# Kernel optimization log

Hardware: AMD Instinct MI355X
Metric: run time of the kernel (lower is better)

## Reference

```python
import jax, jax.numpy as jnp
from jax import lax
import numpy as np

D_STATE = 16
D_CONV = 4
GROUPS = 4
TOKEN = 8


def group_norm(x, w, b, groups, eps=1e-5):
    # x: [B, C, H, W]; torch GroupNorm semantics
    B, C, H, W = x.shape
    xg = x.reshape(B, groups, C // groups, H, W)
    mu = xg.mean(axis=(2, 3, 4), keepdims=True)
    var = ((xg - mu) ** 2).mean(axis=(2, 3, 4), keepdims=True)
    xg = (xg - mu) / jnp.sqrt(var + eps)
    return xg.reshape(B, C, H, W) * w[None, :, None, None] + b[None, :, None, None]


def mamba_fwd(x, in_w, conv_w, conv_b, xproj_w, dt_w, dt_b, A_log, D, out_w):
    # x: [B, L, d_model]. Faithful mamba_ssm Mamba forward (no biases on in/out proj).
    Bsz, L, _ = x.shape
    d_inner = in_w.shape[0] // 2
    dt_rank = dt_w.shape[1]
    xz = x @ in_w.T                                   # [B, L, 2*d_inner]
    xi, z = jnp.split(xz, 2, axis=-1)
    # causal depthwise conv1d (kernel D_CONV) + SiLU
    xc = lax.conv_general_dilated(
        xi.transpose(0, 2, 1), conv_w, window_strides=(1,),
        padding=[(D_CONV - 1, 0)], dimension_numbers=("NCH", "OIH", "NCH"),
        feature_group_count=d_inner)
    xc = jax.nn.silu(xc + conv_b[None, :, None]).transpose(0, 2, 1)  # [B, L, d_inner]
    xdb = xc @ xproj_w.T                               # [B, L, dt_rank + 2*d_state]
    dt, Bm, Cm = jnp.split(xdb, [dt_rank, dt_rank + D_STATE], axis=-1)
    dt = jax.nn.softplus(dt @ dt_w.T + dt_b)           # [B, L, d_inner]
    A = -jnp.exp(A_log)                                # [d_inner, d_state]
    dA = jnp.exp(dt[..., None] * A)                    # [B, L, d_inner, d_state]
    dBx = dt[..., None] * Bm[:, :, None, :] * xc[..., None]

    def step(h, inp):
        dA_t, dBx_t, C_t = inp                         # [B,di,ds],[B,di,ds],[B,ds]
        h = dA_t * h + dBx_t
        y = jnp.einsum('bds,bs->bd', h, C_t)
        return h, y

    h0 = jnp.zeros((Bsz, d_inner, D_STATE), dtype=x.dtype)
    _, ys = lax.scan(step, h0, (dA.transpose(1, 0, 2, 3),
                                dBx.transpose(1, 0, 2, 3),
                                Cm.transpose(1, 0, 2)))
    y = ys.transpose(1, 0, 2) + xc * D                 # skip term D*x
    y = y * jax.nn.silu(z)
    return y @ out_w.T


def setup_inputs() -> dict:
    key = jax.random.key(0)
    ks = iter(jax.random.split(key, 48))

    def rn(shape, s=0.02):
        return jax.random.normal(next(ks), shape, dtype=jnp.float32) * s

    B, C, H, W = 4, 64, 64, 64
    inp = {"x": jax.random.normal(next(ks), (B, C, H, W), dtype=jnp.float32)}

    def mamba_params(prefix, d_model):
        d_inner = 2 * d_model
        dt_rank = -(-d_model // 16)
        inp[prefix + "_in_w"] = rn((2 * d_inner, d_model))
        inp[prefix + "_conv_w"] = rn((d_inner, 1, D_CONV))
        inp[prefix + "_conv_b"] = rn((d_inner,))
        inp[prefix + "_xproj_w"] = rn((dt_rank + 2 * D_STATE, d_inner))
        inp[prefix + "_dt_w"] = rn((d_inner, dt_rank))
        inp[prefix + "_dt_b"] = rn((d_inner,)) + 0.5
        inp[prefix + "_A_log"] = jnp.log(jnp.tile(jnp.arange(1, D_STATE + 1, dtype=jnp.float32), (d_inner, 1)))
        inp[prefix + "_D"] = jnp.ones((d_inner,), jnp.float32)
        inp[prefix + "_out_w"] = rn((d_model, d_inner))

    mamba_params("spa", C)
    mamba_params("spe", -(-C // TOKEN))  # group_channel_num = ceil(64/8) = 8
    inp["spa_gn_w"] = jnp.ones((C,), jnp.float32)
    inp["spa_gn_b"] = jnp.zeros((C,), jnp.float32)
    inp["spe_gn_w"] = jnp.ones((C,), jnp.float32)
    inp["spe_gn_b"] = jnp.zeros((C,), jnp.float32)
    inp["att_w"] = jnp.full((2,), 0.5, jnp.float32)
    return inp


def reference(x,
              spa_in_w, spa_conv_w, spa_conv_b, spa_xproj_w, spa_dt_w, spa_dt_b,
              spa_A_log, spa_D, spa_out_w,
              spe_in_w, spe_conv_w, spe_conv_b, spe_xproj_w, spe_dt_w, spe_dt_b,
              spe_A_log, spe_D, spe_out_w,
              spa_gn_w, spa_gn_b, spe_gn_w, spe_gn_b, att_w):
    B, C, H, W = x.shape
    gcn = -(-C // TOKEN)  # C == TOKEN*gcn here, so no padding path is taken

    # --- SpaMamba: flatten all pixels into one sequence [1, B*H*W, C] ---
    xs = x.transpose(0, 2, 3, 1).reshape(1, -1, C)
    ys = mamba_fwd(xs, spa_in_w, spa_conv_w, spa_conv_b, spa_xproj_w,
                   spa_dt_w, spa_dt_b, spa_A_log, spa_D, spa_out_w)
    ys = ys.reshape(B, H, W, C).transpose(0, 3, 1, 2)
    spa = jax.nn.silu(group_norm(ys, spa_gn_w, spa_gn_b, GROUPS)) + x

    # --- SpeMamba: per-pixel spectral tokens [B*H*W, TOKEN, gcn] ---
    xe = x.transpose(0, 2, 3, 1).reshape(B * H * W, TOKEN, gcn)
    ye = mamba_fwd(xe, spe_in_w, spe_conv_w, spe_conv_b, spe_xproj_w,
                   spe_dt_w, spe_dt_b, spe_A_log, spe_D, spe_out_w)
    ye = ye.reshape(B, H, W, C).transpose(0, 3, 1, 2)
    spe = x + jax.nn.silu(group_norm(ye, spe_gn_w, spe_gn_b, GROUPS))

    w = jax.nn.softmax(att_w)
    return spa * w[0] + spe * w[1] + x
```

## Files before the change

kernel.cpp:

```cpp
#include <hip/hip_runtime.h>

__device__ __forceinline__ float siluf(float x){ return x / (1.f + __expf(-x)); }
__device__ __forceinline__ float softplusf(float x){
    return fmaxf(x, 0.f) + __logf(1.f + __expf(-fabsf(x)));
}
#if __has_builtin(__builtin_amdgcn_exp2f)
__device__ __forceinline__ float fexp2(float x){ return __builtin_amdgcn_exp2f(x); }
#else
__device__ __forceinline__ float fexp2(float x){ return exp2f(x); }
#endif

__global__ void __launch_bounds__(256) k_inproj_conv(const float* __restrict__ x,
        const float* __restrict__ in_w, const float* __restrict__ cw, const float* __restrict__ cb,
        float* __restrict__ xc, float* __restrict__ zb){
    __shared__ float sxe[11][68];
    int tid = threadIdx.x;
    int l0 = blockIdx.x * 8;
    #pragma unroll
    for (int it = 0; it < 3; ++it){
        int idx = it*256 + tid;
        if (idx < 704){
            int r = idx >> 6, c = idx & 63;
            int p = l0 - 3 + r;
            float v = 0.f;
            if (p >= 0) v = x[(size_t)(p >> 12)*262144 + c*4096 + (p & 4095)];
            sxe[r][c] = v;
        }
    }
    float wr[64];
    const float4* w4 = (const float4*)(in_w + tid*64);
    #pragma unroll
    for (int k = 0; k < 16; ++k){
        float4 v = w4[k];
        wr[4*k]=v.x; wr[4*k+1]=v.y; wr[4*k+2]=v.z; wr[4*k+3]=v.w;
    }
    __syncthreads();
    if (tid < 128){
        float acc[11];
        #pragma unroll
        for (int r = 0; r < 11; ++r) acc[r] = 0.f;
        #pragma unroll
        for (int k = 0; k < 16; ++k){
            #pragma unroll
            for (int r = 0; r < 11; ++r){
                float4 v = *(const float4*)&sxe[r][4*k];
                acc[r] = fmaf(v.x, wr[4*k],   acc[r]);
                acc[r] = fmaf(v.y, wr[4*k+1], acc[r]);
                acc[r] = fmaf(v.z, wr[4*k+2], acc[r]);
                acc[r] = fmaf(v.w, wr[4*k+3], acc[r]);
            }
        }
        float cw0 = cw[tid*4+0], cw1 = cw[tid*4+1], cw2 = cw[tid*4+2], cw3 = cw[tid*4+3];
        float cbd = cb[tid];
        #pragma unroll
        for (int r = 0; r < 8; ++r){
            float a = fmaf(cw0, acc[r],   cbd);
            a = fmaf(cw1, acc[r+1], a);
            a = fmaf(cw2, acc[r+2], a);
            a = fmaf(cw3, acc[r+3], a);
            xc[(size_t)(l0+r)*128 + tid] = siluf(a);
        }
    } else {
        float acc[8];
        #pragma unroll
        for (int r = 0; r < 8; ++r) acc[r] = 0.f;
        #pragma unroll
        for (int k = 0; k < 16; ++k){
            #pragma unroll
            for (int r = 0; r < 8; ++r){
                float4 v = *(const float4*)&sxe[r+3][4*k];
                acc[r] = fmaf(v.x, wr[4*k],   acc[r]);
                acc[r] = fmaf(v.y, wr[4*k+1], acc[r]);
                acc[r] = fmaf(v.z, wr[4*k+2], acc[r]);
                acc[r] = fmaf(v.w, wr[4*k+3], acc[r]);
            }
        }
        int dz = tid - 128;
        #pragma unroll
        for (int r = 0; r < 8; ++r) zb[(size_t)(l0+r)*128 + dz] = acc[r];
    }
}

__global__ void __launch_bounds__(256) k_scan_p1(const float* __restrict__ xc,
        const float* __restrict__ xpw, const float* __restrict__ dtw, const float* __restrict__ dtb,
        const float* __restrict__ A_log, float* __restrict__ Pb, float* __restrict__ Qb){
    __shared__ float sxc[2048];
    __shared__ float sbm[256];
    __shared__ __align__(16) float dtr[64];
    const int tid = threadIdx.x;
    const int ch = blockIdx.x;
    {
        const float4* src = (const float4*)(xc + (size_t)ch*2048);
        float4* dst = (float4*)sxc;
        dst[tid] = src[tid];
        dst[256 + tid] = src[256 + tid];
    }
    __syncthreads();
    {
        int j = tid & 63, tg = tid >> 6;
        if (j < 20){
            const float4* w4  = (const float4*)(xpw + j*128);
            const float4* xc4 = (const float4*)sxc + tg*128;
            float acc[4];
            #pragma unroll
            for (int r = 0; r < 4; ++r) acc[r] = 0.f;
            #pragma unroll 8
            for (int k = 0; k < 32; ++k){
                float4 w = w4[k];
                #pragma unroll
                for (int r = 0; r < 4; ++r){
                    float4 v = xc4[r*32 + k];
                    acc[r] = fmaf(v.x, w.x, acc[r]);
                    acc[r] = fmaf(v.y, w.y, acc[r]);
                    acc[r] = fmaf(v.z, w.z, acc[r]);
                    acc[r] = fmaf(v.w, w.w, acc[r]);
                }
            }
            if (j < 4){
                #pragma unroll
                for (int r = 0; r < 4; ++r) dtr[(tg*4+r)*4 + j] = acc[r];
            } else {
                #pragma unroll
                for (int r = 0; r < 4; ++r) sbm[(tg*4+r)*16 + (j-4)] = acc[r];
            }
        }
    }
    __syncthreads();
    const int d  = tid & 127;
    const int sh = tid >> 7;
    float A8[8];
    {
        const float4* al4 = (const float4*)(A_log + d*16 + sh*8);
        float4 v0 = al4[0], v1 = al4[1];
        A8[0]=-__expf(v0.x)*1.44269504f; A8[1]=-__expf(v0.y)*1.44269504f;
        A8[2]=-__expf(v0.z)*1.44269504f; A8[3]=-__expf(v0.w)*1.44269504f;
        A8[4]=-__expf(v1.x)*1.44269504f; A8[5]=-__expf(v1.y)*1.44269504f;
        A8[6]=-__expf(v1.z)*1.44269504f; A8[7]=-__expf(v1.w)*1.44269504f;
    }
    float4 dw = *(const float4*)(dtw + d*4);
    float dbd = dtb[d];
    float P[8], Q[8];
    #pragma unroll
    for (int s = 0; s < 8; ++s){ P[s] = 1.f; Q[s] = 0.f; }
    #pragma unroll 4
    for (int i = 0; i < 16; ++i){
        float4 dt4 = *(const float4*)(dtr + i*4);
        float dv = dbd;
        dv = fmaf(dt4.x, dw.x, dv);
        dv = fmaf(dt4.y, dw.y, dv);
        dv = fmaf(dt4.z, dw.z, dv);
        dv = fmaf(dt4.w, dw.w, dv);
        float dt = softplusf(dv);
        float db = dt * sxc[i*128 + d];
        const float4* bmr = (const float4*)(sbm + i*16 + sh*8);
        float4 b0 = bmr[0], b1 = bmr[1];
        float bv[8] = {b0.x,b0.y,b0.z,b0.w,b1.x,b1.y,b1.z,b1.w};
        #pragma unroll
        for (int s = 0; s < 8; ++s){
            float a = fexp2(dt*A8[s]);
            P[s] *= a;
            Q[s] = fmaf(a, Q[s], db*bv[s]);
        }
    }
    float* Pp = Pb + (size_t)ch*2048 + d*16 + sh*8;
    float* Qp = Qb + (size_t)ch*2048 + d*16 + sh*8;
    ((float4*)Pp)[0] = make_float4(P[0],P[1],P[2],P[3]);
    ((float4*)Pp)[1] = make_float4(P[4],P[5],P[6],P[7]);
    ((float4*)Qp)[0] = make_float4(Q[0],Q[1],Q[2],Q[3]);
    ((float4*)Qp)[1] = make_float4(Q[4],Q[5],Q[6],Q[7]);
}

#define XE_   0
#define XCL_  1216
#define BCL_  3904
#define DTV_  8640
#define SPG_  8768
#define WEIN_ 8800
#define WECW_ 9056
#define WECB_ 9120
#define WEAL_ 9136
#define WDTW_ 9392
#define WDTB_ 9408
#define WDV_  9424
__global__ void __launch_bounds__(256) k_spe(
        const float* __restrict__ x,
        const float* __restrict__ ein_w, const float* __restrict__ ecw, const float* __restrict__ ecb,
        const float* __restrict__ expw, const float* __restrict__ edtw, const float* __restrict__ edtb,
        const float* __restrict__ eA_log, const float* __restrict__ eDv, const float* __restrict__ eow,
        float* __restrict__ ye, float* __restrict__ sp)
{
    __shared__ float smem[9440];
    const int tid = threadIdx.x;
    const int pix = tid >> 4;
    const int d   = tid & 15;
    const int eb  = blockIdx.x;
    const int p0  = eb * 16;
    const int b   = p0 >> 12;
    const int hw0 = p0 & 4095;

    #pragma unroll
    for (int it = 0; it < 3; ++it){
        int idx = it*256 + tid;
        if (idx < 640){
            float v;
            if      (idx < 256) v = ein_w[idx];
            else if (idx < 320) v = ecw[idx-256];
            else if (idx < 336) v = ecb[idx-320];
            else if (idx < 592) v = eA_log[idx-336];
            else if (idx < 608) v = edtw[idx-592];
            else if (idx < 624) v = edtb[idx-608];
            else                v = eDv[idx-624];
            smem[WEIN_ + idx] = v;
        }
    }
    const float* xb = x + b*262144 + hw0;
    #pragma unroll
    for (int it = 0; it < 4; ++it){
        int idx = it*256 + tid;
        smem[XE_ + (idx&15)*76 + (idx>>4)] = xb[(idx>>4)*4096 + (idx&15)];
    }
    __syncthreads();

    float wi[8], wz[8];
    #pragma unroll
    for (int g = 0; g < 8; ++g){ wi[g] = smem[WEIN_ + d*8+g]; wz[g] = smem[WEIN_ + 128 + d*8+g]; }
    float xi[8], zz[8];
    {
        const float4* xe4 = (const float4*)(smem + XE_ + pix*76);
        #pragma unroll
        for (int t = 0; t < 8; ++t){
            float4 a = xe4[t*2], bq = xe4[t*2+1];
            float xv8[8] = {a.x,a.y,a.z,a.w,bq.x,bq.y,bq.z,bq.w};
            float ai = 0.f, az = 0.f;
            #pragma unroll
            for (int g = 0; g < 8; ++g){
                ai = fmaf(xv8[g], wi[g], ai);
                az = fmaf(xv8[g], wz[g], az);
            }
            xi[t] = ai; zz[t] = az;
        }
    }
    float c0 = smem[WECW_ + d*4+0], c1 = smem[WECW_ + d*4+1];
    float c2 = smem[WECW_ + d*4+2], c3 = smem[WECW_ + d*4+3];
    float cbd = smem[WECB_ + d];
    float xcr[8];
    #pragma unroll
    for (int t = 0; t < 8; ++t){
        float a = fmaf(c3, xi[t], cbd);
        if (t >= 1) a = fmaf(c2, xi[t-1], a);
        if (t >= 2) a = fmaf(c1, xi[t-2], a);
        if (t >= 3) a = fmaf(c0, xi[t-3], a);
        xcr[t] = siluf(a);
        smem[XCL_ + pix*168 + t*20 + d] = xcr[t];
    }
    __syncthreads();

    {
        const int row = tid & 127;
        const int jh  = tid >> 7;
        const int px2 = row >> 3;
        const int t2  = row & 7;
        const float4* xr = (const float4*)(smem + XCL_ + px2*168 + t2*20);
        float4 r0 = xr[0], r1 = xr[1], r2 = xr[2], r3 = xr[3];
        float xv[16] = {r0.x,r0.y,r0.z,r0.w, r1.x,r1.y,r1.z,r1.w,
                        r2.x,r2.y,r2.z,r2.w, r3.x,r3.y,r3.z,r3.w};
        const float* wbase = expw + (1 + jh*16)*16;
        float outv[16];
        #pragma unroll
        for (int s = 0; s < 16; ++s){
            const float* wr = wbase + s*16;
            float a = 0.f;
            #pragma unroll
            for (int k = 0; k < 16; ++k) a = fmaf(xv[k], wr[k], a);
            outv[s] = a;
        }
        float4* dst4 = (float4*)(smem + BCL_ + px2*296 + t2*36 + jh*16);
        dst4[0] = make_float4(outv[0], outv[1], outv[2], outv[3]);
        dst4[1] = make_float4(outv[4], outv[5], outv[6], outv[7]);
        dst4[2] = make_float4(outv[8], outv[9], outv[10],outv[11]);
        dst4[3] = make_float4(outv[12],outv[13],outv[14],outv[15]);
        if (jh == 0){
            float accd = 0.f;
            #pragma unroll
            for (int k = 0; k < 16; ++k) accd = fmaf(xv[k], expw[k], accd);
            smem[DTV_ + px2*8 + t2] = accd;
        }
    }
    __syncthreads();

    float A16[16];
    #pragma unroll
    for (int s = 0; s < 16; ++s) A16[s] = -__expf(smem[WEAL_ + d*16+s]) * 1.44269504f;
    float dwd = smem[WDTW_ + d], dbd = smem[WDTB_ + d], Dd = smem[WDV_ + d];
    float h[16];
    #pragma unroll
    for (int s = 0; s < 16; ++s) h[s] = 0.f;
    #pragma unroll
    for (int t = 0; t < 8; ++t){
        float dtd = softplusf(fmaf(smem[DTV_ + pix*8 + t], dwd, dbd));
        float db = dtd * xcr[t];
        const float4* bc4 = (const float4*)(smem + BCL_ + pix*296 + t*36);
        float4 b0 = bc4[0], b1 = bc4[1], b2 = bc4[2], b3 = bc4[3];
        float4 cc0 = bc4[4], cc1 = bc4[5], cc2 = bc4[6], cc3 = bc4[7];
        float bv[16] = {b0.x,b0.y,b0.z,b0.w, b1.x,b1.y,b1.z,b1.w,
                        b2.x,b2.y,b2.z,b2.w, b3.x,b3.y,b3.z,b3.w};
        float cv[16] = {cc0.x,cc0.y,cc0.z,cc0.w, cc1.x,cc1.y,cc1.z,cc1.w,
                        cc2.x,cc2.y,cc2.z,cc2.w, cc3.x,cc3.y,cc3.z,cc3.w};
        float yp = 0.f;
        #pragma unroll
        for (int s = 0; s < 16; ++s){
            float a = fexp2(dtd*A16[s]);
            h[s] = fmaf(a, h[s], db*bv[s]);
            yp = fmaf(h[s], cv[s], yp);
        }
        smem[pix*168 + t*20 + d] = (yp + xcr[t]*Dd) * siluf(zz[t]);
    }
    __syncthreads();

    {
        const int half = tid >> 7;
        const int idx7 = tid & 127;
        const int pixD = idx7 >> 3;
        const int ttD  = idx7 & 7;
        const int m0   = half*4;
        const float4* y4 = (const float4*)(smem + pixD*168 + ttD*20);
        float4 y0 = y4[0], y1 = y4[1], y2 = y4[2], y3 = y4[3];
        float ylr[16] = {y0.x,y0.y,y0.z,y0.w, y1.x,y1.y,y1.z,y1.w,
                         y2.x,y2.y,y2.z,y2.w, y3.x,y3.y,y3.z,y3.w};
        float acc[4];
        #pragma unroll
        for (int mm = 0; mm < 4; ++mm){
            const float* wr = eow + (m0+mm)*16;
            float a = 0.f;
            #pragma unroll
            for (int k = 0; k < 16; ++k) a = fmaf(ylr[k], wr[k], a);
            acc[mm] = a;
        }
        float4 o; o.x=acc[0]; o.y=acc[1]; o.z=acc[2]; o.w=acc[3];
        *(float4*)(ye + (size_t)(p0+pixD)*64 + ttD*8 + m0) = o;

        float s  = acc[0]+acc[1]+acc[2]+acc[3];
        float ss = acc[0]*acc[0]+acc[1]*acc[1]+acc[2]*acc[2]+acc[3]*acc[3];
        s += __shfl_xor(s,1);  ss += __shfl_xor(ss,1);
        s += __shfl_xor(s,8);  ss += __shfl_xor(ss,8);
        s += __shfl_xor(s,16); ss += __shfl_xor(ss,16);
        s += __shfl_xor(s,32); ss += __shfl_xor(ss,32);
        int lane = tid & 63, wv = tid >> 6;
        if ((lane & 57) == 0){
            smem[SPG_ + wv*4 + ((lane>>1)&3)] = s;
            smem[SPG_ + 16 + wv*4 + ((lane>>1)&3)] = ss;
        }
    }
    __syncthreads();
    if (tid < 4){
        int blk = eb & 255;
        float S  = smem[SPG_+0*4+tid]+smem[SPG_+1*4+tid]+smem[SPG_+2*4+tid]+smem[SPG_+3*4+tid];
        float SS = smem[SPG_+16+0*4+tid]+smem[SPG_+16+1*4+tid]+smem[SPG_+16+2*4+tid]+smem[SPG_+16+3*4+tid];
        float* dst = sp + (size_t)(((4 + b)*4 + tid)*512 + blk*2);
        dst[0] = S; dst[1] = SS;
    }
}

__global__ void __launch_bounds__(256) k_scan_p2a(const float* __restrict__ Pb,
        const float* __restrict__ Qb, float* __restrict__ Ps, float* __restrict__ Qs){
    int g = blockIdx.x*256 + threadIdx.x;
    int sup = g >> 11;
    int lane = g & 2047;
    float P = 1.f, Q = 0.f;
    for (int i = 0; i < 64; i += 8){
        float p[8], q[8];
        #pragma unroll
        for (int u = 0; u < 8; ++u){
            p[u] = Pb[(size_t)(sup*64+i+u)*2048 + lane];
            q[u] = Qb[(size_t)(sup*64+i+u)*2048 + lane];
        }
        #pragma unroll
        for (int u = 0; u < 8; ++u){
            P = p[u]*P;
            Q = fmaf(p[u], Q, q[u]);
        }
    }
    Ps[g] = P; Qs[g] = Q;
}

__global__ void __launch_bounds__(256) k_scan_p2c(const float* __restrict__ Pb,
        const float* __restrict__ Qb, const float* __restrict__ Ps,
        const float* __restrict__ Qs, float* __restrict__ Hs){
    int g = blockIdx.x*256 + threadIdx.x;
    int sup = g >> 11;
    int lane = g & 2047;
    float h = 0.f;
    for (int u = 0; u < sup; ++u){
        float p = Ps[u*2048 + lane];
        float q = Qs[u*2048 + lane];
        h = fmaf(p, h, q);
    }
    for (int i = 0; i < 64; i += 8){
        float p[8], q[8];
        #pragma unroll
        for (int u = 0; u < 8; ++u){
            p[u] = Pb[(size_t)(sup*64+i+u)*2048 + lane];
            q[u] = Qb[(size_t)(sup*64+i+u)*2048 + lane];
        }
        #pragma unroll
        for (int u = 0; u < 8; ++u){
            Hs[(size_t)(sup*64+i+u)*2048 + lane] = h;
            h = fmaf(p[u], h, q[u]);
        }
    }
}

__global__ void __launch_bounds__(256) k_scan_p3(const float* __restrict__ xc,
        const float* __restrict__ zb, const float* __restrict__ xpw, const float* __restrict__ dtw,
        const float* __restrict__ dtb, const float* __restrict__ A_log, const float* __restrict__ Dv,
        const float* __restrict__ Hs, const float* __restrict__ ow,
        float* __restrict__ ys, float* __restrict__ sp){
    __shared__ float sxc[16*128];
    __shared__ float ypl[2][16*128];
    __shared__ float sbm[16*16];
    __shared__ float scm[16*16];
    __shared__ __align__(16) float dtr[16][4];
    __shared__ float pgs[2][2][4];
    const int tid = threadIdx.x;
    const int ch = blockIdx.x;
    {
        const float4* src = (const float4*)(xc + (size_t)ch*2048);
        float4* dst = (float4*)sxc;
        dst[tid] = src[tid];
        dst[256 + tid] = src[256 + tid];
    }
    __syncthreads();
    {
        int j = tid & 63, tg = tid >> 6;
        if (j < 36){
            const float4* w4  = (const float4*)(xpw + j*128);
            const float4* xc4 = (const float4*)sxc + tg*128;
            float acc[4];
            #pragma unroll
            for (int r = 0; r < 4; ++r) acc[r] = 0.f;
            #pragma unroll 8
            for (int k = 0; k < 32; ++k){
                float4 w = w4[k];
                #pragma unroll
                for (int r = 0; r < 4; ++r){
                    float4 v = xc4[r*32 + k];
                    acc[r] = fmaf(v.x, w.x, acc[r]);
                    acc[r] = fmaf(v.y, w.y, acc[r]);
                    acc[r] = fmaf(v.z, w.z, acc[r]);
                    acc[r] = fmaf(v.w, w.w, acc[r]);
                }
            }
            if (j < 4){
                #pragma unroll
                for (int r = 0; r < 4; ++r) dtr[tg*4+r][j] = acc[r];
            } else if (j < 20){
                #pragma unroll
                for (int r = 0; r < 4; ++r) sbm[(tg*4+r)*16 + (j-4)] = acc[r];
            } else {
                #pragma unroll
                for (int r = 0; r < 4; ++r) scm[(tg*4+r)*16 + (j-20)] = acc[r];
            }
        }
    }
    __syncthreads();
    const int d  = tid & 127;
    const int sh = tid >> 7;
    float A8[8], h[8];
    {
        const float4* al4 = (const float4*)(A_log + d*16 + sh*8);
        float4 v0 = al4[0], v1 = al4[1];
        A8[0]=-__expf(v0.x)*1.44269504f; A8[1]=-__expf(v0.y)*1.44269504f;
        A8[2]=-__expf(v0.z)*1.44269504f; A8[3]=-__expf(v0.w)*1.44269504f;
        A8[4]=-__expf(v1.x)*1.44269504f; A8[5]=-__expf(v1.y)*1.44269504f;
        A8[6]=-__expf(v1.z)*1.44269504f; A8[7]=-__expf(v1.w)*1.44269504f;
        const float4* h4 = (const float4*)(Hs + (size_t)ch*2048 + d*16 + sh*8);
        float4 h0 = h4[0], h1 = h4[1];
        h[0]=h0.x; h[1]=h0.y; h[2]=h0.z; h[3]=h0.w;
        h[4]=h1.x; h[5]=h1.y; h[6]=h1.z; h[7]=h1.w;
    }
    float4 dw = *(const float4*)(dtw + d*4);
    float dbd = dtb[d];
    #pragma unroll 4
    for (int i = 0; i < 16; ++i){
        float4 dt4 = *(const float4*)dtr[i];
        float dv = dbd;
        dv = fmaf(dt4.x, dw.x, dv);
        dv = fmaf(dt4.y, dw.y, dv);
        dv = fmaf(dt4.z, dw.z, dv);
        dv = fmaf(dt4.w, dw.w, dv);
        float dt = softplusf(dv);
        float db = dt * sxc[i*128 + d];
        const float4* bmr = (const float4*)(sbm + i*16 + sh*8);
        const float4* cmr = (const float4*)(scm + i*16 + sh*8);
        float4 b0 = bmr[0], b1 = bmr[1];
        float4 c0 = cmr[0], c1 = cmr[1];
        float bv[8] = {b0.x,b0.y,b0.z,b0.w,b1.x,b1.y,b1.z,b1.w};
        float cv[8] = {c0.x,c0.y,c0.z,c0.w,c1.x,c1.y,c1.z,c1.w};
        float yp = 0.f;
        #pragma unroll
        for (int s = 0; s < 8; ++s){
            float a = fexp2(dt*A8[s]);
            h[s] = fmaf(a, h[s], db*bv[s]);
            yp = fmaf(h[s], cv[s], yp);
        }
        ypl[sh][i*128 + d] = yp;
    }
    __syncthreads();
    #pragma unroll
    for (int it = 0; it < 8; ++it){
        int idx = it*256 + tid;
        float yp = ypl[0][idx] + ypl[1][idx];
        float xcd = sxc[idx];
        float zv = zb[(size_t)ch*2048 + idx];
        ypl[0][idx] = (yp + xcd*Dv[idx & 127]) * siluf(zv);
    }
    __syncthreads();
    {
        int c  = tid & 63;
        int kh = (tid >> 6) & 1;
        int rg = tid >> 7;
        float wr[64];
        const float4* w4o = (const float4*)(ow + c*128 + kh*64);
        #pragma unroll
        for (int k = 0; k < 16; ++k){
            float4 v = w4o[k];
            wr[4*k]=v.x; wr[4*k+1]=v.y; wr[4*k+2]=v.z; wr[4*k+3]=v.w;
        }
        float acc[8];
        #pragma unroll
        for (int r = 0; r < 8; ++r) acc[r] = 0.f;
        const float4* y4 = (const float4*)(ypl[0] + rg*8*128 + kh*64);
        #pragma unroll
        for (int k = 0; k < 16; ++k){
            #pragma unroll
            for (int r = 0; r < 8; ++r){
                float4 v = y4[r*32 + k];
                acc[r] = fmaf(v.x, wr[4*k],   acc[r]);
                acc[r] = fmaf(v.y, wr[4*k+1], acc[r]);
                acc[r] = fmaf(v.z, wr[4*k+2], acc[r]);
                acc[r] = fmaf(v.w, wr[4*k+3], acc[r]);
            }
        }
        float* part = ypl[1];
        if (kh == 1){
            #pragma unroll
            for (int r = 0; r < 8; ++r) part[(rg*8+r)*64 + c] = acc[r];
        }
        __syncthreads();
        if (kh == 0){
            float s = 0.f, ss = 0.f;
            #pragma unroll
            for (int r = 0; r < 8; ++r){
                float v = acc[r] + part[(rg*8+r)*64 + c];
                ys[(size_t)(ch*16 + rg*8 + r)*64 + c] = v;
                s += v; ss += v*v;
            }
            s += __shfl_xor(s,1); ss += __shfl_xor(ss,1);
            s += __shfl_xor(s,2); ss += __shfl_xor(ss,2);
            s += __shfl_xor(s,4); ss += __shfl_xor(ss,4);
            s += __shfl_xor(s,8); ss += __shfl_xor(ss,8);
            if ((c & 15) == 0){ pgs[0][rg][c>>4] = s; pgs[1][rg][c>>4] = ss; }
        }
        __syncthreads();
        if (tid < 4){
            int b = ch >> 8, blk = ch & 255;
            float S  = pgs[0][0][tid] + pgs[0][1][tid];
            float SS = pgs[1][0][tid] + pgs[1][1][tid];
            float* dst = sp + (size_t)((b*4 + tid)*512 + blk*2);
            dst[0] = S; dst[1] = SS;
        }
    }
}

__global__ void __launch_bounds__(256) k_final(const float* __restrict__ x,
        const float* __restrict__ ys, const float* __restrict__ ye,
        const float* __restrict__ sp,
        const float* __restrict__ gsw, const float* __restrict__ gsb,
        const float* __restrict__ gew, const float* __restrict__ geb,
        const float* __restrict__ attw, float* __restrict__ out){
    __shared__ float st[16];
    __shared__ float tys[32][65];
    __shared__ float tye[32][65];
    int tid = threadIdx.x;
    int b   = blockIdx.x >> 7;
    int hw0 = (blockIdx.x & 127) << 5;
    {
        int combo = tid >> 5;
        int j = tid & 31;
        int t = combo >> 2, g = combo & 3;
        const float4* bp = (const float4*)(sp + (size_t)(t*16 + b*4 + g)*512 + j*16);
        float s = 0.f, ss = 0.f;
        #pragma unroll
        for (int k = 0; k < 4; ++k){ float4 v = bp[k]; s += v.x+v.z; ss += v.y+v.w; }
        s += __shfl_xor(s,1);  ss += __shfl_xor(ss,1);
        s += __shfl_xor(s,2);  ss += __shfl_xor(ss,2);
        s += __shfl_xor(s,4);  ss += __shfl_xor(ss,4);
        s += __shfl_xor(s,8);  ss += __shfl_xor(ss,8);
        s += __shfl_xor(s,16); ss += __shfl_xor(ss,16);
        if (j == 0){
            float m = s * (1.f/65536.f);
            float v = ss * (1.f/65536.f) - m*m;
            st[combo*2]   = m;
            st[combo*2+1] = rsqrtf(v + 1e-5f);
        }
    }
    const float* ysb = ys + ((size_t)(b*4096 + hw0))*64;
    const float* yeb = ye + ((size_t)(b*4096 + hw0))*64;
    #pragma unroll
    for (int it = 0; it < 8; ++it){
        int idx = it*256 + tid;
        tys[idx>>6][idx&63] = ysb[idx];
        tye[idx>>6][idx&63] = yeb[idx];
    }
    __syncthreads();
    float a0 = attw[0], a1 = attw[1];
    float mx = fmaxf(a0, a1);
    float e0 = __expf(a0-mx), e1 = __expf(a1-mx);
    float inv = 1.f/(e0+e1);
    float w0 = e0*inv, w1 = e1*inv;
    #pragma unroll
    for (int it = 0; it < 8; ++it){
        int idx = it*256 + tid;
        int c = idx >> 5, hwi = idx & 31;
        int g = c >> 4;
        size_t gx = ((size_t)(b*64 + c))*4096 + hw0 + hwi;
        float xv = x[gx];
        float ns = (tys[hwi][c] - st[g*2])     * st[g*2+1]     * gsw[c] + gsb[c];
        float ne = (tye[hwi][c] - st[8+g*2])   * st[8+g*2+1]   * gew[c] + geb[c];
        out[gx] = w0*(siluf(ns)+xv) + w1*(xv+siluf(ne)) + xv;
    }
}

#define OFF_YS 0u
#define OFF_XC 1048832u
#define OFF_Z  3145984u
#define OFF_PB 5243136u
#define OFF_QB 7340288u
#define OFF_HS 9437440u
#define OFF_YE 11534592u
#define OFF_PS 12583168u
#define OFF_QS 12615936u
#define OFF_SP 12648704u

extern "C" void kernel_launch(void* const* d_in, const int* in_sizes, int n_in,
                              void* d_out, int out_size, void* d_ws, size_t ws_size,
                              hipStream_t stream) {
    const float* x           = (const float*)d_in[0];
    const float* spa_in_w    = (const float*)d_in[1];
    const float* spa_conv_w  = (const float*)d_in[2];
    const float* spa_conv_b  = (const float*)d_in[3];
    const float* spa_xproj_w = (const float*)d_in[4];
    const float* spa_dt_w    = (const float*)d_in[5];
    const float* spa_dt_b    = (const float*)d_in[6];
    const float* spa_A_log   = (const float*)d_in[7];
    const float* spa_D       = (const float*)d_in[8];
    const float* spa_out_w   = (const float*)d_in[9];
    const float* spe_in_w    = (const float*)d_in[10];
    const float* spe_conv_w  = (const float*)d_in[11];
    const float* spe_conv_b  = (const float*)d_in[12];
    const float* spe_xproj_w = (const float*)d_in[13];
    const float* spe_dt_w    = (const float*)d_in[14];
    const float* spe_dt_b    = (const float*)d_in[15];
    const float* spe_A_log   = (const float*)d_in[16];
    const float* spe_D       = (const float*)d_in[17];
    const float* spe_out_w   = (const float*)d_in[18];
    const float* spa_gn_w    = (const float*)d_in[19];
    const float* spa_gn_b    = (const float*)d_in[20];
    const float* spe_gn_w    = (const float*)d_in[21];
    const float* spe_gn_b    = (const float*)d_in[22];
    const float* att_w       = (const float*)d_in[23];

    float* ws  = (float*)d_ws;
    float* xc  = ws + OFF_XC;
    float* zb  = ws + OFF_Z;
    float* Pb  = ws + OFF_PB;
    float* Qb  = ws + OFF_QB;
    float* Hs  = ws + OFF_HS;
    float* Ps  = ws + OFF_PS;
    float* Qs  = ws + OFF_QS;
    float* sp  = ws + OFF_SP;
    float* ysb = ws + OFF_YS;
    float* yeb = ws + OFF_YE;
    float* out = (float*)d_out;

    k_inproj_conv<<<2048, 256, 0, stream>>>(x, spa_in_w, spa_conv_w, spa_conv_b, xc, zb);
    k_scan_p1    <<<1024, 256, 0, stream>>>(xc, spa_xproj_w, spa_dt_w, spa_dt_b, spa_A_log,
                                            Pb, Qb);
    k_spe        <<<1024, 256, 0, stream>>>(x, spe_in_w, spe_conv_w, spe_conv_b, spe_xproj_w,
                                            spe_dt_w, spe_dt_b, spe_A_log, spe_D, spe_out_w,
                                            yeb, sp);
    k_scan_p2a   <<<128,  256, 0, stream>>>(Pb, Qb, Ps, Qs);
    k_scan_p2c   <<<128,  256, 0, stream>>>(Pb, Qb, Ps, Qs, Hs);
    k_scan_p3    <<<1024, 256, 0, stream>>>(xc, zb, spa_xproj_w, spa_dt_w, spa_dt_b,
                                            spa_A_log, spa_D, Hs, spa_out_w, ysb, sp);
    k_final      <<<512,  256, 0, stream>>>(x, ysb, yeb, sp, spa_gn_w, spa_gn_b,
                                            spe_gn_w, spe_gn_b, att_w, out);
}
```

Baseline: 118.4 us.

## Fuse in-projection/conv kernel into scan phase-1 kernel via shared memory

Merges the in-projection plus causal conv kernel into the first scan-phase kernel. Each block now computes its 16-token chunk of xc in two 8-token passes and writes it straight into shared memory, so phase 1 no longer has to reload xc from global memory. This removes one kernel launch and a global round trip for xc, though xc is still written out for the later phase-3 kernel. In exchange, the in-projection runs on half as many blocks, with serialized passes and extra barriers, and shared memory per block grows.

```diff
diff --git a/kernel.cpp b/kernel.cpp
--- a/kernel.cpp
+++ b/kernel.cpp
@@ -10,92 +10,93 @@
 __device__ __forceinline__ float fexp2(float x){ return exp2f(x); }
 #endif
 
-__global__ void __launch_bounds__(256) k_inproj_conv(const float* __restrict__ x,
+__global__ void __launch_bounds__(256) k_ip1(const float* __restrict__ x,
         const float* __restrict__ in_w, const float* __restrict__ cw, const float* __restrict__ cb,
-        float* __restrict__ xc, float* __restrict__ zb){
-    __shared__ float sxe[11][68];
-    int tid = threadIdx.x;
-    int l0 = blockIdx.x * 8;
-    #pragma unroll
-    for (int it = 0; it < 3; ++it){
-        int idx = it*256 + tid;
-        if (idx < 704){
-            int r = idx >> 6, c = idx & 63;
-            int p = l0 - 3 + r;
-            float v = 0.f;
-            if (p >= 0) v = x[(size_t)(p >> 12)*262144 + c*4096 + (p & 4095)];
-            sxe[r][c] = v;
-        }
-    }
-    float wr[64];
-    const float4* w4 = (const float4*)(in_w + tid*64);
-    #pragma unroll
-    for (int k = 0; k < 16; ++k){
-        float4 v = w4[k];
-        wr[4*k]=v.x; wr[4*k+1]=v.y; wr[4*k+2]=v.z; wr[4*k+3]=v.w;
-    }
-    __syncthreads();
-    if (tid < 128){
-        float acc[11];
-        #pragma unroll
-        for (int r = 0; r < 11; ++r) acc[r] = 0.f;
-        #pragma unroll
-        for (int k = 0; k < 16; ++k){
-            #pragma unroll
-            for (int r = 0; r < 11; ++r){
-                float4 v = *(const float4*)&sxe[r][4*k];
-                acc[r] = fmaf(v.x, wr[4*k],   acc[r]);
-                acc[r] = fmaf(v.y, wr[4*k+1], acc[r]);
-                acc[r] = fmaf(v.z, wr[4*k+2], acc[r]);
-                acc[r] = fmaf(v.w, wr[4*k+3], acc[r]);
-            }
-        }
-        float cw0 = cw[tid*4+0], cw1 = cw[tid*4+1], cw2 = cw[tid*4+2], cw3 = cw[tid*4+3];
-        float cbd = cb[tid];
-        #pragma unroll
-        for (int r = 0; r < 8; ++r){
-            float a = fmaf(cw0, acc[r],   cbd);
-            a = fmaf(cw1, acc[r+1], a);
-            a = fmaf(cw2, acc[r+2], a);
-            a = fmaf(cw3, acc[r+3], a);
-            xc[(size_t)(l0+r)*128 + tid] = siluf(a);
-        }
-    } else {
-        float acc[8];
-        #pragma unroll
-        for (int r = 0; r < 8; ++r) acc[r] = 0.f;
-        #pragma unroll
-        for (int k = 0; k < 16; ++k){
-            #pragma unroll
-            for (int r = 0; r < 8; ++r){
-                float4 v = *(const float4*)&sxe[r+3][4*k];
-                acc[r] = fmaf(v.x, wr[4*k],   acc[r]);
-                acc[r] = fmaf(v.y, wr[4*k+1], acc[r]);
-                acc[r] = fmaf(v.z, wr[4*k+2], acc[r]);
-                acc[r] = fmaf(v.w, wr[4*k+3], acc[r]);
-            }
-        }
-        int dz = tid - 128;
-        #pragma unroll
-        for (int r = 0; r < 8; ++r) zb[(size_t)(l0+r)*128 + dz] = acc[r];
-    }
-}
-
-__global__ void __launch_bounds__(256) k_scan_p1(const float* __restrict__ xc,
         const float* __restrict__ xpw, const float* __restrict__ dtw, const float* __restrict__ dtb,
-        const float* __restrict__ A_log, float* __restrict__ Pb, float* __restrict__ Qb){
+        const float* __restrict__ A_log,
+        float* __restrict__ xc, float* __restrict__ zb,
+        float* __restrict__ Pb, float* __restrict__ Qb){
     __shared__ float sxc[2048];
     __shared__ float sbm[256];
     __shared__ __align__(16) float dtr[64];
+    __shared__ float sxe[11][68];
     const int tid = threadIdx.x;
     const int ch = blockIdx.x;
     {
-        const float4* src = (const float4*)(xc + (size_t)ch*2048);
-        float4* dst = (float4*)sxc;
-        dst[tid] = src[tid];
-        dst[256 + tid] = src[256 + tid];
-    }
-    __syncthreads();
+        float wr[64];
+        const float4* w4 = (const float4*)(in_w + tid*64);
+        #pragma unroll
+        for (int k = 0; k < 16; ++k){
+            float4 v = w4[k];
+            wr[4*k]=v.x; wr[4*k+1]=v.y; wr[4*k+2]=v.z; wr[4*k+3]=v.w;
+        }
+        float cw0=0.f,cw1=0.f,cw2=0.f,cw3=0.f,cbd=0.f;
+        if (tid < 128){
+            cw0 = cw[tid*4+0]; cw1 = cw[tid*4+1];
+            cw2 = cw[tid*4+2]; cw3 = cw[tid*4+3];
+            cbd = cb[tid];
+        }
+        for (int pass = 0; pass < 2; ++pass){
+            int l0 = ch*16 + pass*8;
+            #pragma unroll
+            for (int it = 0; it < 3; ++it){
+                int idx = it*256 + tid;
+                if (idx < 704){
+                    int r = idx >> 6, c = idx & 63;
+                    int p = l0 - 3 + r;
+                    float v = 0.f;
+                    if (p >= 0) v = x[(size_t)(p >> 12)*262144 + c*4096 + (p & 4095)];
+                    sxe[r][c] = v;
+                }
+            }
+            __syncthreads();
+            if (tid < 128){
+                float acc[11];
+                #pragma unroll
+                for (int r = 0; r < 11; ++r) acc[r] = 0.f;
+                #pragma unroll
+                for (int k = 0; k < 16; ++k){
+                    #pragma unroll
+                    for (int r = 0; r < 11; ++r){
+                        float4 v = *(const float4*)&sxe[r][4*k];
+                        acc[r] = fmaf(v.x, wr[4*k],   acc[r]);
+                        acc[r] = fmaf(v.y, wr[4*k+1], acc[r]);
+                        acc[r] = fmaf(v.z, wr[4*k+2], acc[r]);
+                        acc[r] = fmaf(v.w, wr[4*k+3], acc[r]);
+                    }
+                }
+                #pragma unroll
+                for (int r = 0; r < 8; ++r){
+                    float a = fmaf(cw0, acc[r],   cbd);
+                    a = fmaf(cw1, acc[r+1], a);
+                    a = fmaf(cw2, acc[r+2], a);
+                    a = fmaf(cw3, acc[r+3], a);
+                    float v = siluf(a);
+                    sxc[(pass*8+r)*128 + tid] = v;
+                    xc[(size_t)(l0+r)*128 + tid] = v;
+                }
+            } else {
+                float acc[8];
+                #pragma unroll
+                for (int r = 0; r < 8; ++r) acc[r] = 0.f;
+                #pragma unroll
+                for (int k = 0; k < 16; ++k){
+                    #pragma unroll
+                    for (int r = 0; r < 8; ++r){
+                        float4 v = *(const float4*)&sxe[r+3][4*k];
+                        acc[r] = fmaf(v.x, wr[4*k],   acc[r]);
+                        acc[r] = fmaf(v.y, wr[4*k+1], acc[r]);
+                        acc[r] = fmaf(v.z, wr[4*k+2], acc[r]);
+                        acc[r] = fmaf(v.w, wr[4*k+3], acc[r]);
+                    }
+                }
+                int dz = tid - 128;
+                #pragma unroll
+                for (int r = 0; r < 8; ++r) zb[(size_t)(l0+r)*128 + dz] = acc[r];
+            }
+            __syncthreads();
+        }
+    }
     {
         int j = tid & 63, tg = tid >> 6;
         if (j < 20){
@@ -683,16 +684,16 @@
     float* yeb = ws + OFF_YE;
     float* out = (float*)d_out;
 
-    k_inproj_conv<<<2048, 256, 0, stream>>>(x, spa_in_w, spa_conv_w, spa_conv_b, xc, zb);
-    k_scan_p1    <<<1024, 256, 0, stream>>>(xc, spa_xproj_w, spa_dt_w, spa_dt_b, spa_A_log,
-                                            Pb, Qb);
-    k_spe        <<<1024, 256, 0, stream>>>(x, spe_in_w, spe_conv_w, spe_conv_b, spe_xproj_w,
-                                            spe_dt_w, spe_dt_b, spe_A_log, spe_D, spe_out_w,
-                                            yeb, sp);
-    k_scan_p2a   <<<128,  256, 0, stream>>>(Pb, Qb, Ps, Qs);
-    k_scan_p2c   <<<128,  256, 0, stream>>>(Pb, Qb, Ps, Qs, Hs);
-    k_scan_p3    <<<1024, 256, 0, stream>>>(xc, zb, spa_xproj_w, spa_dt_w, spa_dt_b,
-                                            spa_A_log, spa_D, Hs, spa_out_w, ysb, sp);
-    k_final      <<<512,  256, 0, stream>>>(x, ysb, yeb, sp, spa_gn_w, spa_gn_b,
-                                            spe_gn_w, spe_gn_b, att_w, out);
-}
+    k_ip1     <<<1024, 256, 0, stream>>>(x, spa_in_w, spa_conv_w, spa_conv_b,
+                                         spa_xproj_w, spa_dt_w, spa_dt_b, spa_A_log,
+                                         xc, zb, Pb, Qb);
+    k_spe     <<<1024, 256, 0, stream>>>(x, spe_in_w, spe_conv_w, spe_conv_b, spe_xproj_w,
+                                         spe_dt_w, spe_dt_b, spe_A_log, spe_D, spe_out_w,
+                                         yeb, sp);
+    k_scan_p2a<<<128,  256, 0, stream>>>(Pb, Qb, Ps, Qs);
+    k_scan_p2c<<<128,  256, 0, stream>>>(Pb, Qb, Ps, Qs, Hs);
+    k_scan_p3 <<<1024, 256, 0, stream>>>(xc, zb, spa_xproj_w, spa_dt_w, spa_dt_b,
+                                         spa_A_log, spa_D, Hs, spa_out_w, ysb, sp);
+    k_final   <<<512,  256, 0, stream>>>(x, ysb, yeb, sp, spa_gn_w, spa_gn_b,
+                                         spe_gn_w, spe_gn_b, att_w, out);
+}
```

After: 115.0 us, median of 3. 1.03x faster.
